# Optimization experiments

Hardware: AMD Instinct MI355X
Metric: run time of the kernel (lower is better)

## Reference

```python
import jax, jax.numpy as jnp
import numpy as np

J, F_ = 17, 32  # joints x per-joint features; C = J*F_ = 544
H = 8           # num_heads
EPS = 1e-5


def _layernorm(x, g, b):
    mu = jnp.mean(x, axis=-1, keepdims=True)
    var = jnp.mean((x - mu) ** 2, axis=-1, keepdims=True)
    return (x - mu) * jax.lax.rsqrt(var + EPS) * g + b


def setup_inputs() -> dict:
    key = jax.random.key(0)
    ks = jax.random.split(key, 8)
    B, N, C = 8, 1024, J * F_
    x = jax.random.normal(ks[0], (B, N, C), dtype=jnp.float32)
    s = 1.0 / np.sqrt(C)
    return {
        "x": x,
        "norm_g": jnp.ones((F_,), jnp.float32),
        "norm_b": jnp.zeros((F_,), jnp.float32),
        "ap_w": jax.random.normal(ks[1], (1, F_), jnp.float32) / np.sqrt(F_),
        "ap_b": jnp.zeros((1,), jnp.float32),
        "norm2_g": jnp.ones((C,), jnp.float32),
        "norm2_b": jnp.zeros((C,), jnp.float32),
        "qkv_w": jax.random.normal(ks[2], (3 * C, C), jnp.float32) * s,
        "proj_w": jax.random.normal(ks[3], (C, C), jnp.float32) * s,
        "proj_b": jnp.zeros((C,), jnp.float32),
        "scaling_factor": jnp.array([2.0], jnp.float32),
    }


def reference(x, norm_g, norm_b, ap_w, ap_b, norm2_g, norm2_b, qkv_w, proj_w, proj_b, scaling_factor):
    B, N, C = x.shape
    hd = C // H
    # --- attention pooling over joints ---
    xr = x.reshape(B, N, J, F_)
    xr = _layernorm(xr, norm_g, norm_b)                      # [B,N,17,32]
    scores = jnp.einsum('bnjf,of->bnjo', xr, ap_w)[..., 0] + ap_b[0]  # [B,N,17]
    # nn.Softmax(dim=1): softmax over sequence axis N (faithful to source)
    w = jax.nn.softmax(scores, axis=1)
    xp = (xr * w[..., None]).reshape(B, N, C)
    xp = _layernorm(xp, norm2_g, norm2_b)
    # --- position-scaled self-attention ---
    positions = jnp.linspace(0.0, 1.0, N, dtype=jnp.float32)  # [N]
    pos_scale = jnp.exp(-scaling_factor[0] * (positions - 0.5) ** 2)  # per-key scale
    qkv = (xp @ qkv_w.T).reshape(B, N, 3, H, hd)
    q = qkv[:, :, 0].transpose(0, 2, 1, 3)  # [B,H,N,hd]
    k = qkv[:, :, 1].transpose(0, 2, 1, 3)
    v = qkv[:, :, 2].transpose(0, 2, 1, 3)
    scale = hd ** -0.5
    attn = jnp.einsum('bhqd,bhkd->bhqk', q, k) * (scale * pos_scale[None, None, None, :])
    attn = jax.nn.softmax(attn, axis=-1)
    out = jnp.einsum('bhqk,bhkd->bhqd', attn, v)
    out = out.transpose(0, 2, 1, 3).reshape(B, N, C)
    return out @ proj_w.T + proj_b
```

## Files before the change

### kernel.cpp

```cpp
#include <hip/hip_runtime.h>
#include <hip/hip_bf16.h>

#define BB 8
#define NN 1024
#define CC 544
#define JJ 17
#define FF 32
#define HH 8
#define HD 68
#define BN 8192
#define KD 544
#define NCQ 1632
#define NCQP 1664
#define NCPP 640
#define HDP 96
#define AQR 64

using f32x4  = __attribute__((ext_vector_type(4))) float;
using bf16x8 = __attribute__((ext_vector_type(8))) short;

__device__ __forceinline__ void gld_lds16(const void* g, void* l) {
  __builtin_amdgcn_global_load_lds(
      (const __attribute__((address_space(1))) void*)g,
      (__attribute__((address_space(3))) void*)l, 16, 0, 0);
}

__global__ __launch_bounds__(256) void wconv(const float* __restrict__ qkv_w,
                                             const float* __restrict__ proj_w,
                                             __hip_bfloat16* __restrict__ qw,
                                             __hip_bfloat16* __restrict__ pw,
                                             char* __restrict__ qkp) {
  int bid = blockIdx.x, t = threadIdx.x;
  if (bid < NCQP + NCPP) {
    bool isq = bid < NCQP;
    int r = isq ? bid : bid - NCQP;
    const float* src = isq ? qkv_w : proj_w;
    __hip_bfloat16* dst = isq ? qw : pw;
    int nrows = isq ? NCQ : CC;
    if (t < KD / 4) {
      int c = t * 4;
      float4 v;
      if (r < nrows) v = *(const float4*)(src + (size_t)r * KD + c);
      else           v = float4{0.f, 0.f, 0.f, 0.f};
      __hip_bfloat16 o[4] = {__float2bfloat16(v.x), __float2bfloat16(v.y),
                             __float2bfloat16(v.z), __float2bfloat16(v.w)};
      *(unsigned long long*)(dst + (size_t)r * KD + c) = *(unsigned long long*)o;
    }
  } else {
    int row = (bid - (NCQP + NCPP)) * 256 + t;
    if (row < 131072) {
      char* p = qkp + (size_t)row * 192 + 136;
#pragma unroll
      for (int i = 0; i < 7; ++i) *(unsigned long long*)(p + i * 8) = 0ull;
    }
  }
}

__global__ __launch_bounds__(256) void ln1_scores(const float* __restrict__ x,
                                                  const float* __restrict__ g,
                                                  const float* __restrict__ bta,
                                                  const float* __restrict__ apw,
                                                  const float* __restrict__ apb,
                                                  __hip_bfloat16* __restrict__ xr,
                                                  float* __restrict__ scores) {
  int wv = threadIdx.x >> 6, lane = threadIdx.x & 63;
  int bn = blockIdx.x * 4 + wv;
  int f = lane & 31, half = lane >> 5;
  const float* row = x + (size_t)bn * CC;
  float gg = g[f], bb = bta[f], aw = apw[f], ab = apb[0];
  for (int it = 0; it < 9; ++it) {
    int j = it * 2 + half;
    bool act = (j < JJ);
    float v = act ? row[j * FF + f] : 0.f;
    float s = v;
    for (int m = 16; m >= 1; m >>= 1) s += __shfl_xor(s, m);
    float mu = s * (1.f / 32.f);
    float dv = v - mu;
    float s2 = dv * dv;
    for (int m = 16; m >= 1; m >>= 1) s2 += __shfl_xor(s2, m);
    float xn = dv * rsqrtf(s2 * (1.f / 32.f) + 1e-5f) * gg + bb;
    float sc = xn * aw;
    for (int m = 16; m >= 1; m >>= 1) sc += __shfl_xor(sc, m);
    if (act) {
      xr[(size_t)bn * CC + j * FF + f] = __float2bfloat16(xn);
      if (f == 0) scores[bn * JJ + j] = sc + ab;
    }
  }
}

__global__ __launch_bounds__(256) void softmax_red(const float* __restrict__ scores,
                                                   float2* __restrict__ tab) {
  int bj = blockIdx.x;
  int b = bj / JJ, j = bj - b * JJ;
  const float* s = scores + (size_t)b * NN * JJ + j;
  int t = threadIdx.x;
  float v[4];
  float mx = -1e30f;
#pragma unroll
  for (int i = 0; i < 4; ++i) { v[i] = s[(t + 256 * i) * JJ]; mx = fmaxf(mx, v[i]); }
#pragma unroll
  for (int m = 32; m >= 1; m >>= 1) mx = fmaxf(mx, __shfl_xor(mx, m));
  __shared__ float red[4];
  if ((t & 63) == 0) red[t >> 6] = mx;
  __syncthreads();
  mx = fmaxf(fmaxf(red[0], red[1]), fmaxf(red[2], red[3]));
  float sum = 0.f;
#pragma unroll
  for (int i = 0; i < 4; ++i) sum += __expf(v[i] - mx);
#pragma unroll
  for (int m = 32; m >= 1; m >>= 1) sum += __shfl_xor(sum, m);
  __shared__ float red2[4];
  if ((t & 63) == 0) red2[t >> 6] = sum;
  __syncthreads();
  if (t == 0) {
    sum = red2[0] + red2[1] + red2[2] + red2[3];
    tab[bj] = make_float2(mx, 1.f / sum);
  }
}

__global__ __launch_bounds__(256) void ln2_xp(const __hip_bfloat16* __restrict__ xr,
                                              const float* __restrict__ scores,
                                              const float2* __restrict__ tab,
                                              const float* __restrict__ g2,
                                              const float* __restrict__ b2,
                                              __hip_bfloat16* __restrict__ xp) {
  __shared__ float wsh[4][JJ];
  int wv = threadIdx.x >> 6, lane = threadIdx.x & 63;
  int bn = blockIdx.x * 4 + wv;
  if (lane < JJ) {
    float sc = scores[bn * JJ + lane];
    float2 mi = tab[(bn >> 10) * JJ + lane];
    wsh[wv][lane] = __expf(sc - mi.x) * mi.y;
  }
  float vals[9];
  float sum = 0.f;
  for (int it = 0; it < 9; ++it) {
    int c = it * 64 + lane;
    float v = 0.f;
    if (c < CC) v = __bfloat162float(xr[(size_t)bn * CC + c]) * wsh[wv][c >> 5];
    vals[it] = v;
    sum += v;
  }
  for (int m = 32; m >= 1; m >>= 1) sum += __shfl_xor(sum, m);
  float mu = sum * (1.f / 544.f);
  float s2 = 0.f;
  for (int it = 0; it < 9; ++it) {
    int c = it * 64 + lane;
    if (c < CC) { float dv = vals[it] - mu; s2 += dv * dv; }
  }
  for (int m = 32; m >= 1; m >>= 1) s2 += __shfl_xor(s2, m);
  float rstd = rsqrtf(s2 * (1.f / 544.f) + 1e-5f);
  for (int it = 0; it < 9; ++it) {
    int c = it * 64 + lane;
    if (c < CC)
      xp[(size_t)bn * CC + c] = __float2bfloat16((vals[it] - mu) * rstd * g2[c] + b2[c]);
  }
}

template <int MODE>
__global__ __launch_bounds__(256) void gemm_nt(const __hip_bfloat16* __restrict__ A,
                                               const __hip_bfloat16* __restrict__ Bw,
                                               __hip_bfloat16* __restrict__ Qp,
                                               __hip_bfloat16* __restrict__ Kp,
                                               __hip_bfloat16* __restrict__ Vt,
                                               float* __restrict__ Cf,
                                               const float* __restrict__ bias,
                                               const float* __restrict__ sfp) {
  __shared__ __hip_bfloat16 As[2][128 * 32];
  __shared__ __hip_bfloat16 Bs[2][128 * 32];
  const int t = threadIdx.x;
  const int w = t >> 6, lane = t & 63;
  const int fr = lane & 15, fq = lane >> 4;
  const int bi = blockIdx.x;
  const int xcd = bi & 7, j = bi >> 3;
  const int bx = xcd * 8 + (j & 7), by = j >> 3;
  const int m0 = bx * 128;
  const int n0 = by * 128;
  const int wm = (w >> 1) * 64, wn = (w & 1) * 64;

  f32x4 acc[4][4] = {};

  const __hip_bfloat16* Ag = A + (size_t)m0 * KD;
  const __hip_bfloat16* Bg = Bw + (size_t)n0 * KD;

#pragma unroll
  for (int i2 = 0; i2 < 2; ++i2) {
    int cb = (i2 * 4 + w) * 64;
    int chunk = cb + lane;
    int row = chunk >> 2, c16 = chunk & 3;
    gld_lds16(Ag + (size_t)row * KD + c16 * 8, &As[0][cb * 8]);
    gld_lds16(Bg + (size_t)row * KD + c16 * 8, &Bs[0][cb * 8]);
  }
  __syncthreads();

  for (int kt = 0; kt < 17; ++kt) {
    const int cur = kt & 1;
    if (kt < 16) {
      const int k0 = (kt + 1) * 32;
#pragma unroll
      for (int i2 = 0; i2 < 2; ++i2) {
        int cb = (i2 * 4 + w) * 64;
        int chunk = cb + lane;
        int row = chunk >> 2, c16 = chunk & 3;
        gld_lds16(Ag + (size_t)row * KD + k0 + c16 * 8, &As[1 - cur][cb * 8]);
        gld_lds16(Bg + (size_t)row * KD + k0 + c16 * 8, &Bs[1 - cur][cb * 8]);
      }
    }
    bf16x8 af[4], bfr[4];
#pragma unroll
    for (int tm = 0; tm < 4; ++tm)
      af[tm] = *(const bf16x8*)&As[cur][(wm + tm * 16 + fr) * 32 + fq * 8];
#pragma unroll
    for (int tn = 0; tn < 4; ++tn)
      bfr[tn] = *(const bf16x8*)&Bs[cur][(wn + tn * 16 + fr) * 32 + fq * 8];
#pragma unroll
    for (int tm = 0; tm < 4; ++tm)
#pragma unroll
      for (int tn = 0; tn < 4; ++tn)
        acc[tm][tn] = __builtin_amdgcn_mfma_f32_16x16x32_bf16(af[tm], bfr[tn], acc[tm][tn], 0, 0, 0);
    __syncthreads();
  }

  if (MODE == 1) {
#pragma unroll
    for (int tn = 0; tn < 4; ++tn) {
      int o = n0 + wn + tn * 16 + fr;
      if (o < CC) {
        float bb = bias[o];
#pragma unroll
        for (int tm = 0; tm < 4; ++tm) {
          int m = m0 + wm + tm * 16 + fq * 4;
#pragma unroll
          for (int r = 0; r < 4; ++r)
            Cf[(size_t)(m + r) * CC + o] = acc[tm][tn][r] + bb;
        }
      }
    }
  } else {
    int b = m0 >> 10;
    float sf = sfp[0];
#pragma unroll
    for (int tn = 0; tn < 4; ++tn) {
      int o = n0 + wn + tn * 16 + fr;
      if (o < 2 * CC) {
        bool is_k = (o >= CC);
        int oo = is_k ? o - CC : o;
        int h = oo / HD;
        int d = oo - h * HD;
        __hip_bfloat16* base = is_k ? Kp : Qp;
        __hip_bfloat16* dst = base + ((size_t)(b * HH + h) * NN) * HDP + d;
#pragma unroll
        for (int tm = 0; tm < 4; ++tm) {
          int m = m0 + wm + tm * 16 + fq * 4;
          int n = m & (NN - 1);
#pragma unroll
          for (int r = 0; r < 4; ++r) {
            float v = acc[tm][tn][r];
            if (is_k) {
              float pos = (n + r) * (1.f / 1023.f) - 0.5f;
              v *= __expf(-sf * pos * pos) * 0.12126781251816650f;
            }
            dst[(size_t)(n + r) * HDP] = __float2bfloat16(v);
          }
        }
      } else if (o < NCQ) {
        int oo = o - 2 * CC;
        int h = oo / HD;
        int d = oo - h * HD;
        __hip_bfloat16* vrow = Vt + (((size_t)b * HH + h) * HD + d) * NN;
#pragma unroll
        for (int tm = 0; tm < 4; ++tm) {
          int m = m0 + wm + tm * 16 + fq * 4;
          int n = m & (NN - 1);
#pragma unroll
          for (int r = 0; r < 4; ++r)
            vrow[n + r] = __float2bfloat16(acc[tm][tn][r]);
        }
      }
    }
  }
}

__global__ __launch_bounds__(128) void attn_kernel(const __hip_bfloat16* __restrict__ Qp,
                                                   const __hip_bfloat16* __restrict__ Kp,
                                                   const __hip_bfloat16* __restrict__ Vt,
                                                   __hip_bfloat16* __restrict__ Ao) {
  __shared__ __hip_bfloat16 Qs[12 * 64 * 8];
  __shared__ __hip_bfloat16 Ks[2][12 * 64 * 8];
  const int t = threadIdx.x;
  const int w = t >> 6, lane = t & 63;
  const int fr = lane & 15, fq = lane >> 4;
  const int idx = blockIdx.x;
  const int bh = idx & 63, qt = idx >> 6;
  const int h = bh & 7, b = bh >> 3;

  const __hip_bfloat16* qtile = Qp + ((size_t)bh * NN + qt * AQR) * HDP;
  const __hip_bfloat16* kbase = Kp + (size_t)bh * NN * HDP;
  const __hip_bfloat16* vbase = Vt + (size_t)bh * HD * NN;

#pragma unroll
  for (int i = 0; i < 6; ++i) {
    int kb = i * 2 + w;
    gld_lds16(qtile + (size_t)lane * HDP + kb * 8, &Qs[kb * 64 * 8]);
  }
#pragma unroll
  for (int i = 0; i < 6; ++i) {
    int kb = i * 2 + w;
    gld_lds16(kbase + (size_t)lane * HDP + kb * 8, &Ks[0][kb * 64 * 8]);
  }
  __syncthreads();
  bf16x8 qa[2][3];
#pragma unroll
  for (int g = 0; g < 2; ++g)
#pragma unroll
    for (int ks = 0; ks < 3; ++ks)
      qa[g][ks] = *(const bf16x8*)&Qs[((ks * 4 + fq) * 64 + w * 32 + g * 16 + fr) * 8];
  __syncthreads();

  f32x4 o_acc[2][5] = {};
  float l_part[2][4] = {};
  const int dclamp = (fr < 4) ? 0 : 1;

  for (int kt = 0; kt < 16; ++kt) {
    const int cur = kt & 1;
    bf16x8 vfrag[5][2];
#pragma unroll
    for (int tv = 0; tv < 5; ++tv) {
      int d = tv * 16 + fr;
      int dc = (tv == 4 && dclamp) ? 0 : d;
#pragma unroll
      for (int ks2 = 0; ks2 < 2; ++ks2)
        vfrag[tv][ks2] = *(const bf16x8*)(vbase + (size_t)dc * NN + kt * 64 + ks2 * 32 + fq * 8);
    }
    if (kt < 15) {
      const __hip_bfloat16* ktile = kbase + (size_t)(kt + 1) * 64 * HDP;
#pragma unroll
      for (int i = 0; i < 6; ++i) {
        int kb = i * 2 + w;
        gld_lds16(ktile + (size_t)lane * HDP + kb * 8, &Ks[1 - cur][kb * 64 * 8]);
      }
    }

    f32x4 s[2][4] = {};
#pragma unroll
    for (int tn = 0; tn < 4; ++tn) {
#pragma unroll
      for (int ks = 0; ks < 3; ++ks) {
        bf16x8 kb = *(const bf16x8*)&Ks[cur][((ks * 4 + fq) * 64 + tn * 16 + fr) * 8];
        s[0][tn] = __builtin_amdgcn_mfma_f32_16x16x32_bf16(qa[0][ks], kb, s[0][tn], 0, 0, 0);
        s[1][tn] = __builtin_amdgcn_mfma_f32_16x16x32_bf16(qa[1][ks], kb, s[1][tn], 0, 0, 0);
      }
    }
#pragma unroll
    for (int g = 0; g < 2; ++g) {
      __hip_bfloat16* Pw = &Qs[(w * 2 + g) * 1152];
#pragma unroll
      for (int tn = 0; tn < 4; ++tn)
#pragma unroll
        for (int r = 0; r < 4; ++r) {
          float p = __expf(s[g][tn][r]);
          l_part[g][r] += p;
          Pw[(fq * 4 + r) * 72 + tn * 16 + fr] = __float2bfloat16(p);
        }
    }
#pragma unroll
    for (int ks2 = 0; ks2 < 2; ++ks2) {
      bf16x8 pa0 = *(const bf16x8*)&Qs[(w * 2 + 0) * 1152 + fr * 72 + ks2 * 32 + fq * 8];
      bf16x8 pa1 = *(const bf16x8*)&Qs[(w * 2 + 1) * 1152 + fr * 72 + ks2 * 32 + fq * 8];
#pragma unroll
      for (int tv = 0; tv < 5; ++tv) {
        o_acc[0][tv] = __builtin_amdgcn_mfma_f32_16x16x32_bf16(pa0, vfrag[tv][ks2], o_acc[0][tv], 0, 0, 0);
        o_acc[1][tv] = __builtin_amdgcn_mfma_f32_16x16x32_bf16(pa1, vfrag[tv][ks2], o_acc[1][tv], 0, 0, 0);
      }
    }
    __syncthreads();
  }
#pragma unroll
  for (int g = 0; g < 2; ++g) {
    __hip_bfloat16* obase = Ao + (size_t)(b * NN + qt * AQR + w * 32 + g * 16) * CC + h * HD;
    float inv[4];
#pragma unroll
    for (int r = 0; r < 4; ++r) {
      float l = l_part[g][r];
#pragma unroll
      for (int msk = 8; msk >= 1; msk >>= 1) l += __shfl_xor(l, msk);
      inv[r] = 1.f / l;
    }
#pragma unroll
    for (int tv = 0; tv < 5; ++tv) {
      int d = tv * 16 + fr;
      if (d < HD) {
#pragma unroll
        for (int r = 0; r < 4; ++r)
          obase[(size_t)(fq * 4 + r) * CC + d] = __float2bfloat16(o_acc[g][tv][r] * inv[r]);
      }
    }
  }
}

extern "C" void kernel_launch(void* const* d_in, const int* in_sizes, int n_in,
                              void* d_out, int out_size, void* d_ws, size_t ws_size,
                              hipStream_t stream) {
  (void)in_sizes; (void)n_in; (void)out_size; (void)ws_size;
  const float* x       = (const float*)d_in[0];
  const float* norm_g  = (const float*)d_in[1];
  const float* norm_b  = (const float*)d_in[2];
  const float* ap_w    = (const float*)d_in[3];
  const float* ap_b    = (const float*)d_in[4];
  const float* norm2_g = (const float*)d_in[5];
  const float* norm2_b = (const float*)d_in[6];
  const float* qkv_w   = (const float*)d_in[7];
  const float* proj_w  = (const float*)d_in[8];
  const float* proj_b  = (const float*)d_in[9];
  const float* sf      = (const float*)d_in[10];
  float* out = (float*)d_out;
  char* ws = (char*)d_ws;

  __hip_bfloat16* xr   = (__hip_bfloat16*)(ws);
  float* scores        = (float*)(ws + 8912896);
  float2* tab          = (float2*)(ws + 9469952);
  __hip_bfloat16* xp   = (__hip_bfloat16*)(ws + 9474048);
  __hip_bfloat16* qw   = (__hip_bfloat16*)(ws + 18386944);
  __hip_bfloat16* pw   = (__hip_bfloat16*)(ws + 20197376);
  __hip_bfloat16* vt   = (__hip_bfloat16*)(ws + 20893696);
  __hip_bfloat16* ao   = (__hip_bfloat16*)(ws + 29806592);
  __hip_bfloat16* qp   = (__hip_bfloat16*)(ws + 38719488);
  __hip_bfloat16* kp   = (__hip_bfloat16*)(ws + 51302400);

  wconv<<<NCQP + NCPP + 512, 256, 0, stream>>>(qkv_w, proj_w, qw, pw, (char*)qp);
  ln1_scores<<<BN / 4, 256, 0, stream>>>(x, norm_g, norm_b, ap_w, ap_b, xr, scores);
  softmax_red<<<BB * JJ, 256, 0, stream>>>(scores, tab);
  ln2_xp<<<BN / 4, 256, 0, stream>>>(xr, scores, tab, norm2_g, norm2_b, xp);
  gemm_nt<0><<<dim3(64 * 13), 256, 0, stream>>>(xp, qw, qp, kp, vt, nullptr, nullptr, sf);
  attn_kernel<<<dim3((NN / AQR) * HH * BB), 128, 0, stream>>>(qp, kp, vt, ao);
  gemm_nt<1><<<dim3(64 * 5), 256, 0, stream>>>(ao, pw, nullptr, nullptr, nullptr, out, proj_b, nullptr);
}
```

Before: 224.3 us.

## Shrink Q/K head padding, use four waves per attention block, fold log2e into K

```diff
diff --git a/kernel.cpp b/kernel.cpp
--- a/kernel.cpp
+++ b/kernel.cpp
@@ -13,7 +13,7 @@
 #define NCQ 1632
 #define NCQP 1664
 #define NCPP 640
-#define HDP 96
+#define HDP 80
 #define AQR 64
 
 using f32x4  = __attribute__((ext_vector_type(4))) float;
@@ -49,9 +49,9 @@
   } else {
     int row = (bid - (NCQP + NCPP)) * 256 + t;
     if (row < 131072) {
-      char* p = qkp + (size_t)row * 192 + 136;
-#pragma unroll
-      for (int i = 0; i < 7; ++i) *(unsigned long long*)(p + i * 8) = 0ull;
+      char* p = qkp + (size_t)row * (HDP * 2) + 136;
+#pragma unroll
+      for (int i = 0; i < 3; ++i) *(unsigned long long*)(p + i * 8) = 0ull;
     }
   }
 }
@@ -258,7 +258,7 @@
             float v = acc[tm][tn][r];
             if (is_k) {
               float pos = (n + r) * (1.f / 1023.f) - 0.5f;
-              v *= __expf(-sf * pos * pos) * 0.12126781251816650f;
+              v *= __expf(-sf * pos * pos) * (0.12126781251816650f * 1.44269504088896340f);
             }
             dst[(size_t)(n + r) * HDP] = __float2bfloat16(v);
           }
@@ -281,12 +281,13 @@
   }
 }
 
-__global__ __launch_bounds__(128) void attn_kernel(const __hip_bfloat16* __restrict__ Qp,
-                                                   const __hip_bfloat16* __restrict__ Kp,
-                                                   const __hip_bfloat16* __restrict__ Vt,
-                                                   __hip_bfloat16* __restrict__ Ao) {
-  __shared__ __hip_bfloat16 Qs[12 * 64 * 8];
-  __shared__ __hip_bfloat16 Ks[2][12 * 64 * 8];
+__global__ __launch_bounds__(256, 4) void attn_kernel(const __hip_bfloat16* __restrict__ Qp,
+                                                      const __hip_bfloat16* __restrict__ Kp,
+                                                      const __hip_bfloat16* __restrict__ Vt,
+                                                      __hip_bfloat16* __restrict__ Ao) {
+  __shared__ __hip_bfloat16 Ps[5120];
+  __shared__ __hip_bfloat16 Ks[2][10 * 64 * 8];
+  __shared__ __hip_bfloat16 Zs[64 * 8];
   const int t = threadIdx.x;
   const int w = t >> 6, lane = t & 63;
   const int fr = lane & 15, fq = lane >> 4;
@@ -298,27 +299,31 @@
   const __hip_bfloat16* kbase = Kp + (size_t)bh * NN * HDP;
   const __hip_bfloat16* vbase = Vt + (size_t)bh * HD * NN;
 
-#pragma unroll
-  for (int i = 0; i < 6; ++i) {
-    int kb = i * 2 + w;
-    gld_lds16(qtile + (size_t)lane * HDP + kb * 8, &Qs[kb * 64 * 8]);
-  }
-#pragma unroll
-  for (int i = 0; i < 6; ++i) {
-    int kb = i * 2 + w;
-    gld_lds16(kbase + (size_t)lane * HDP + kb * 8, &Ks[0][kb * 64 * 8]);
+  if (t < 128) *(unsigned long long*)&Zs[t * 4] = 0ull;
+#pragma unroll
+  for (int i = 0; i < 3; ++i) {
+    int kb = i * 4 + w;
+    if (kb < 10) gld_lds16(qtile + (size_t)lane * HDP + kb * 8, &Ps[kb * 64 * 8]);
+  }
+#pragma unroll
+  for (int i = 0; i < 3; ++i) {
+    int kb = i * 4 + w;
+    if (kb < 10) gld_lds16(kbase + (size_t)lane * HDP + kb * 8, &Ks[0][kb * 64 * 8]);
   }
   __syncthreads();
-  bf16x8 qa[2][3];
-#pragma unroll
-  for (int g = 0; g < 2; ++g)
-#pragma unroll
-    for (int ks = 0; ks < 3; ++ks)
-      qa[g][ks] = *(const bf16x8*)&Qs[((ks * 4 + fq) * 64 + w * 32 + g * 16 + fr) * 8];
+  bf16x8 qa[3];
+#pragma unroll
+  for (int ks = 0; ks < 3; ++ks) {
+    int kblk = ks * 4 + fq;
+    const __hip_bfloat16* qsrc = (ks < 2 || fq < 2)
+        ? &Ps[((size_t)kblk * 64 + w * 16 + fr) * 8]
+        : &Zs[(size_t)(w * 16 + fr) * 8];
+    qa[ks] = *(const bf16x8*)qsrc;
+  }
   __syncthreads();
 
-  f32x4 o_acc[2][5] = {};
-  float l_part[2][4] = {};
+  f32x4 o_acc[5] = {};
+  float l_part[4] = {};
   const int dclamp = (fr < 4) ? 0 : 1;
 
   for (int kt = 0; kt < 16; ++kt) {
@@ -335,65 +340,59 @@
     if (kt < 15) {
       const __hip_bfloat16* ktile = kbase + (size_t)(kt + 1) * 64 * HDP;
 #pragma unroll
-      for (int i = 0; i < 6; ++i) {
-        int kb = i * 2 + w;
-        gld_lds16(ktile + (size_t)lane * HDP + kb * 8, &Ks[1 - cur][kb * 64 * 8]);
-      }
-    }
-
-    f32x4 s[2][4] = {};
+      for (int i = 0; i < 3; ++i) {
+        int kb = i * 4 + w;
+        if (kb < 10) gld_lds16(ktile + (size_t)lane * HDP + kb * 8, &Ks[1 - cur][kb * 64 * 8]);
+      }
+    }
+
+    f32x4 s[4] = {};
 #pragma unroll
     for (int tn = 0; tn < 4; ++tn) {
 #pragma unroll
       for (int ks = 0; ks < 3; ++ks) {
-        bf16x8 kb = *(const bf16x8*)&Ks[cur][((ks * 4 + fq) * 64 + tn * 16 + fr) * 8];
-        s[0][tn] = __builtin_amdgcn_mfma_f32_16x16x32_bf16(qa[0][ks], kb, s[0][tn], 0, 0, 0);
-        s[1][tn] = __builtin_amdgcn_mfma_f32_16x16x32_bf16(qa[1][ks], kb, s[1][tn], 0, 0, 0);
-      }
-    }
-#pragma unroll
-    for (int g = 0; g < 2; ++g) {
-      __hip_bfloat16* Pw = &Qs[(w * 2 + g) * 1152];
-#pragma unroll
-      for (int tn = 0; tn < 4; ++tn)
-#pragma unroll
-        for (int r = 0; r < 4; ++r) {
-          float p = __expf(s[g][tn][r]);
-          l_part[g][r] += p;
-          Pw[(fq * 4 + r) * 72 + tn * 16 + fr] = __float2bfloat16(p);
-        }
-    }
+        int kblk = ks * 4 + fq;
+        const __hip_bfloat16* ksrc = (ks < 2 || fq < 2)
+            ? &Ks[cur][((size_t)kblk * 64 + tn * 16 + fr) * 8]
+            : &Zs[(size_t)(tn * 16 + fr) * 8];
+        bf16x8 kb = *(const bf16x8*)ksrc;
+        s[tn] = __builtin_amdgcn_mfma_f32_16x16x32_bf16(qa[ks], kb, s[tn], 0, 0, 0);
+      }
+    }
+    __hip_bfloat16* Pw = &Ps[w * 1152];
+#pragma unroll
+    for (int tn = 0; tn < 4; ++tn)
+#pragma unroll
+      for (int r = 0; r < 4; ++r) {
+        float p = __builtin_amdgcn_exp2f(s[tn][r]);
+        l_part[r] += p;
+        Pw[(fq * 4 + r) * 72 + tn * 16 + fr] = __float2bfloat16(p);
+      }
 #pragma unroll
     for (int ks2 = 0; ks2 < 2; ++ks2) {
-      bf16x8 pa0 = *(const bf16x8*)&Qs[(w * 2 + 0) * 1152 + fr * 72 + ks2 * 32 + fq * 8];
-      bf16x8 pa1 = *(const bf16x8*)&Qs[(w * 2 + 1) * 1152 + fr * 72 + ks2 * 32 + fq * 8];
-#pragma unroll
-      for (int tv = 0; tv < 5; ++tv) {
-        o_acc[0][tv] = __builtin_amdgcn_mfma_f32_16x16x32_bf16(pa0, vfrag[tv][ks2], o_acc[0][tv], 0, 0, 0);
-        o_acc[1][tv] = __builtin_amdgcn_mfma_f32_16x16x32_bf16(pa1, vfrag[tv][ks2], o_acc[1][tv], 0, 0, 0);
-      }
+      bf16x8 pa = *(const bf16x8*)&Ps[w * 1152 + fr * 72 + ks2 * 32 + fq * 8];
+#pragma unroll
+      for (int tv = 0; tv < 5; ++tv)
+        o_acc[tv] = __builtin_amdgcn_mfma_f32_16x16x32_bf16(pa, vfrag[tv][ks2], o_acc[tv], 0, 0, 0);
     }
     __syncthreads();
   }
-#pragma unroll
-  for (int g = 0; g < 2; ++g) {
-    __hip_bfloat16* obase = Ao + (size_t)(b * NN + qt * AQR + w * 32 + g * 16) * CC + h * HD;
-    float inv[4];
-#pragma unroll
-    for (int r = 0; r < 4; ++r) {
-      float l = l_part[g][r];
-#pragma unroll
-      for (int msk = 8; msk >= 1; msk >>= 1) l += __shfl_xor(l, msk);
-      inv[r] = 1.f / l;
-    }
-#pragma unroll
-    for (int tv = 0; tv < 5; ++tv) {
-      int d = tv * 16 + fr;
-      if (d < HD) {
-#pragma unroll
-        for (int r = 0; r < 4; ++r)
-          obase[(size_t)(fq * 4 + r) * CC + d] = __float2bfloat16(o_acc[g][tv][r] * inv[r]);
-      }
+  __hip_bfloat16* obase = Ao + (size_t)(b * NN + qt * AQR + w * 16) * CC + h * HD;
+  float inv[4];
+#pragma unroll
+  for (int r = 0; r < 4; ++r) {
+    float l = l_part[r];
+#pragma unroll
+    for (int msk = 8; msk >= 1; msk >>= 1) l += __shfl_xor(l, msk);
+    inv[r] = 1.f / l;
+  }
+#pragma unroll
+  for (int tv = 0; tv < 5; ++tv) {
+    int d = tv * 16 + fr;
+    if (d < HD) {
+#pragma unroll
+      for (int r = 0; r < 4; ++r)
+        obase[(size_t)(fq * 4 + r) * CC + d] = __float2bfloat16(o_acc[tv][r] * inv[r]);
     }
   }
 }
@@ -425,13 +424,13 @@
   __hip_bfloat16* vt   = (__hip_bfloat16*)(ws + 20893696);
   __hip_bfloat16* ao   = (__hip_bfloat16*)(ws + 29806592);
   __hip_bfloat16* qp   = (__hip_bfloat16*)(ws + 38719488);
-  __hip_bfloat16* kp   = (__hip_bfloat16*)(ws + 51302400);
+  __hip_bfloat16* kp   = (__hip_bfloat16*)(ws + 49205248);
 
   wconv<<<NCQP + NCPP + 512, 256, 0, stream>>>(qkv_w, proj_w, qw, pw, (char*)qp);
   ln1_scores<<<BN / 4, 256, 0, stream>>>(x, norm_g, norm_b, ap_w, ap_b, xr, scores);
   softmax_red<<<BB * JJ, 256, 0, stream>>>(scores, tab);
   ln2_xp<<<BN / 4, 256, 0, stream>>>(xr, scores, tab, norm2_g, norm2_b, xp);
   gemm_nt<0><<<dim3(64 * 13), 256, 0, stream>>>(xp, qw, qp, kp, vt, nullptr, nullptr, sf);
-  attn_kernel<<<dim3((NN / AQR) * HH * BB), 128, 0, stream>>>(qp, kp, vt, ao);
+  attn_kernel<<<dim3((NN / AQR) * HH * BB), 256, 0, stream>>>(qp, kp, vt, ao);
   gemm_nt<1><<<dim3(64 * 5), 256, 0, stream>>>(ao, pw, nullptr, nullptr, nullptr, out, proj_b, nullptr);
 }
```

After: 247.6 us. 1.1x slower.

## Store Q/K in blocked 8-wide d-chunk layout and use exp2 in attention

Applied to the files above, without the earlier changes.

```diff
diff --git a/kernel.cpp b/kernel.cpp
--- a/kernel.cpp
+++ b/kernel.cpp
@@ -13,7 +13,8 @@
 #define NCQ 1632
 #define NCQP 1664
 #define NCPP 640
-#define HDP 96
+#define NKB 9
+#define BHSZ 73728
 #define AQR 64
 
 using f32x4  = __attribute__((ext_vector_type(4))) float;
@@ -49,9 +50,9 @@
   } else {
     int row = (bid - (NCQP + NCPP)) * 256 + t;
     if (row < 131072) {
-      char* p = qkp + (size_t)row * 192 + 136;
-#pragma unroll
-      for (int i = 0; i < 7; ++i) *(unsigned long long*)(p + i * 8) = 0ull;
+      int bhT = row >> 10, n = row & 1023;
+      char* p = qkp + (size_t)bhT * 147456 + 131072 + (size_t)n * 16 + 8;
+      *(unsigned long long*)p = 0ull;
     }
   }
 }
@@ -248,7 +249,7 @@
         int h = oo / HD;
         int d = oo - h * HD;
         __hip_bfloat16* base = is_k ? Kp : Qp;
-        __hip_bfloat16* dst = base + ((size_t)(b * HH + h) * NN) * HDP + d;
+        __hip_bfloat16* dst = base + (size_t)(b * HH + h) * BHSZ + (d >> 3) * (NN * 8) + (d & 7);
 #pragma unroll
         for (int tm = 0; tm < 4; ++tm) {
           int m = m0 + wm + tm * 16 + fq * 4;
@@ -258,9 +259,9 @@
             float v = acc[tm][tn][r];
             if (is_k) {
               float pos = (n + r) * (1.f / 1023.f) - 0.5f;
-              v *= __expf(-sf * pos * pos) * 0.12126781251816650f;
+              v *= __expf(-sf * pos * pos) * (0.12126781251816650f * 1.44269504088896340f);
             }
-            dst[(size_t)(n + r) * HDP] = __float2bfloat16(v);
+            dst[(size_t)(n + r) * 8] = __float2bfloat16(v);
           }
         }
       } else if (o < NCQ) {
@@ -285,8 +286,9 @@
                                                    const __hip_bfloat16* __restrict__ Kp,
                                                    const __hip_bfloat16* __restrict__ Vt,
                                                    __hip_bfloat16* __restrict__ Ao) {
-  __shared__ __hip_bfloat16 Qs[12 * 64 * 8];
-  __shared__ __hip_bfloat16 Ks[2][12 * 64 * 8];
+  __shared__ __hip_bfloat16 Qs[NKB * 64 * 8];
+  __shared__ __hip_bfloat16 Ks[2][NKB * 64 * 8];
+  __shared__ __hip_bfloat16 Zs[64 * 8];
   const int t = threadIdx.x;
   const int w = t >> 6, lane = t & 63;
   const int fr = lane & 15, fq = lane >> 4;
@@ -294,27 +296,30 @@
   const int bh = idx & 63, qt = idx >> 6;
   const int h = bh & 7, b = bh >> 3;
 
-  const __hip_bfloat16* qtile = Qp + ((size_t)bh * NN + qt * AQR) * HDP;
-  const __hip_bfloat16* kbase = Kp + (size_t)bh * NN * HDP;
+  const __hip_bfloat16* qtile = Qp + (size_t)bh * BHSZ + (size_t)qt * AQR * 8;
+  const __hip_bfloat16* kbase = Kp + (size_t)bh * BHSZ;
   const __hip_bfloat16* vbase = Vt + (size_t)bh * HD * NN;
 
-#pragma unroll
-  for (int i = 0; i < 6; ++i) {
+  *(unsigned long long*)&Zs[t * 4] = 0ull;
+#pragma unroll
+  for (int i = 0; i < 5; ++i) {
     int kb = i * 2 + w;
-    gld_lds16(qtile + (size_t)lane * HDP + kb * 8, &Qs[kb * 64 * 8]);
-  }
-#pragma unroll
-  for (int i = 0; i < 6; ++i) {
+    if (kb < NKB) gld_lds16(qtile + (size_t)kb * (NN * 8) + lane * 8, &Qs[kb * 64 * 8]);
+  }
+#pragma unroll
+  for (int i = 0; i < 5; ++i) {
     int kb = i * 2 + w;
-    gld_lds16(kbase + (size_t)lane * HDP + kb * 8, &Ks[0][kb * 64 * 8]);
+    if (kb < NKB) gld_lds16(kbase + (size_t)kb * (NN * 8) + lane * 8, &Ks[0][kb * 64 * 8]);
   }
   __syncthreads();
   bf16x8 qa[2][3];
 #pragma unroll
-  for (int g = 0; g < 2; ++g)
-#pragma unroll
-    for (int ks = 0; ks < 3; ++ks)
-      qa[g][ks] = *(const bf16x8*)&Qs[((ks * 4 + fq) * 64 + w * 32 + g * 16 + fr) * 8];
+  for (int ks = 0; ks < 3; ++ks) {
+    const __hip_bfloat16* qb = (ks < 2 || fq == 0) ? &Qs[(ks * 4 + fq) * 64 * 8] : Zs;
+#pragma unroll
+    for (int g = 0; g < 2; ++g)
+      qa[g][ks] = *(const bf16x8*)&qb[(w * 32 + g * 16 + fr) * 8];
+  }
   __syncthreads();
 
   f32x4 o_acc[2][5] = {};
@@ -333,20 +338,21 @@
         vfrag[tv][ks2] = *(const bf16x8*)(vbase + (size_t)dc * NN + kt * 64 + ks2 * 32 + fq * 8);
     }
     if (kt < 15) {
-      const __hip_bfloat16* ktile = kbase + (size_t)(kt + 1) * 64 * HDP;
-#pragma unroll
-      for (int i = 0; i < 6; ++i) {
+      const __hip_bfloat16* ktile = kbase + (size_t)(kt + 1) * 64 * 8;
+#pragma unroll
+      for (int i = 0; i < 5; ++i) {
         int kb = i * 2 + w;
-        gld_lds16(ktile + (size_t)lane * HDP + kb * 8, &Ks[1 - cur][kb * 64 * 8]);
+        if (kb < NKB) gld_lds16(ktile + (size_t)kb * (NN * 8) + lane * 8, &Ks[1 - cur][kb * 64 * 8]);
       }
     }
 
     f32x4 s[2][4] = {};
 #pragma unroll
-    for (int tn = 0; tn < 4; ++tn) {
-#pragma unroll
-      for (int ks = 0; ks < 3; ++ks) {
-        bf16x8 kb = *(const bf16x8*)&Ks[cur][((ks * 4 + fq) * 64 + tn * 16 + fr) * 8];
+    for (int ks = 0; ks < 3; ++ks) {
+      const __hip_bfloat16* kbL = (ks < 2 || fq == 0) ? &Ks[cur][(ks * 4 + fq) * 64 * 8] : Zs;
+#pragma unroll
+      for (int tn = 0; tn < 4; ++tn) {
+        bf16x8 kb = *(const bf16x8*)&kbL[(tn * 16 + fr) * 8];
         s[0][tn] = __builtin_amdgcn_mfma_f32_16x16x32_bf16(qa[0][ks], kb, s[0][tn], 0, 0, 0);
         s[1][tn] = __builtin_amdgcn_mfma_f32_16x16x32_bf16(qa[1][ks], kb, s[1][tn], 0, 0, 0);
       }
@@ -358,7 +364,7 @@
       for (int tn = 0; tn < 4; ++tn)
 #pragma unroll
         for (int r = 0; r < 4; ++r) {
-          float p = __expf(s[g][tn][r]);
+          float p = __builtin_amdgcn_exp2f(s[g][tn][r]);
           l_part[g][r] += p;
           Pw[(fq * 4 + r) * 72 + tn * 16 + fr] = __float2bfloat16(p);
         }
@@ -425,7 +431,7 @@
   __hip_bfloat16* vt   = (__hip_bfloat16*)(ws + 20893696);
   __hip_bfloat16* ao   = (__hip_bfloat16*)(ws + 29806592);
   __hip_bfloat16* qp   = (__hip_bfloat16*)(ws + 38719488);
-  __hip_bfloat16* kp   = (__hip_bfloat16*)(ws + 51302400);
+  __hip_bfloat16* kp   = (__hip_bfloat16*)(ws + 48156672);
 
   wconv<<<NCQP + NCPP + 512, 256, 0, stream>>>(qkv_w, proj_w, qw, pw, (char*)qp);
   ln1_scores<<<BN / 4, 256, 0, stream>>>(x, norm_g, norm_b, ap_w, ap_b, xr, scores);
```

Measured after the change: 218.5 us. -2.6%, faster.
